# Kernel tuning notes

Measured on AMD Instinct MI355X. Metric: run time of the kernel, lower is better.

Reference implementation:

```python
import jax, jax.numpy as jnp
import numpy as np

EPS = 1e-5


def setup_inputs() -> dict:
    key = jax.random.key(0)
    ks = jax.random.split(key, 6)
    b, n, x_len, h_len = 128, 512, 512, 512
    fan_in = x_len + h_len
    std = float(np.sqrt(2.0 / fan_in))  # kaiming_normal_ for [h_len, x_len+h_len]
    X = jax.random.normal(ks[0], (b, n, x_len), dtype=jnp.float32)
    W_a = jax.random.normal(ks[1], (h_len, fan_in), dtype=jnp.float32) * std
    W_g = jax.random.normal(ks[2], (h_len, fan_in), dtype=jnp.float32) * std
    b_a = jax.random.normal(ks[3], (h_len,), dtype=jnp.float32) * 0.02
    b_g = jax.random.normal(ks[4], (h_len,), dtype=jnp.float32) * 0.02
    gamma = jnp.ones((h_len,), dtype=jnp.float32)
    beta = jnp.zeros((h_len,), dtype=jnp.float32)
    return {"X": X, "W_a": W_a, "W_g": W_g, "b_a": b_a, "b_g": b_g,
            "gamma": gamma, "beta": beta}


def _layernorm(x, gamma, beta):
    mu = jnp.mean(x, axis=-1, keepdims=True)
    var = jnp.mean(jnp.square(x - mu), axis=-1, keepdims=True)
    return (x - mu) * jax.lax.rsqrt(var + EPS) * gamma + beta


def reference(X, W_a, W_g, b_a, b_g, gamma, beta):
    # X: [b, n, x_len]; recurrent scan over the time axis n.
    b, n, x_len = X.shape
    h_len = W_a.shape[0]

    def step(h, x_t):
        cat = jnp.concatenate([h, x_t], axis=-1)          # [b, h+x]
        alpha = jax.nn.sigmoid(cat @ W_g.T + b_g)          # [b, h]
        a = cat @ W_a.T + b_a                              # [b, h]
        h_tilde = alpha * jnp.tanh(a) + (1.0 - alpha) * a  # affine blend
        h_new = _layernorm(h_tilde, gamma, beta)           # dropout = identity (eval)
        return h_new, h_new

    h0 = jnp.zeros((b, h_len), dtype=X.dtype)
    _, ys = jax.lax.scan(step, h0, jnp.swapaxes(X, 0, 1))  # ys: [n, b, h]
    return jnp.swapaxes(ys, 0, 1)                          # [b, n, h]
```

## Files before the change

kernel.cpp:

```cpp
#include <hip/hip_runtime.h>
#include <math.h>

typedef _Float16 f16;
typedef _Float16 f16x8 __attribute__((ext_vector_type(8)));
typedef float f32x4 __attribute__((ext_vector_type(4)));
typedef unsigned long long u64;
typedef unsigned u32;

union U32H2 { unsigned u; f16 h[2]; };
union UV4H8 { uint4 u; f16x8 h; f16 e[8]; };

#define LN_EPS 1e-5f

__device__ __forceinline__ void st_u64g(u64* p, u64 v) {
    __hip_atomic_store(p, v, __ATOMIC_RELAXED, __HIP_MEMORY_SCOPE_AGENT);
}
__device__ __forceinline__ u64 ld_u64g(const u64* p) {
    return __hip_atomic_load(p, __ATOMIC_RELAXED, __HIP_MEMORY_SCOPE_AGENT);
}

__global__ __launch_bounds__(256) void init_ex(u64* p, int n) {
    const int i = blockIdx.x * 256 + threadIdx.x;
    if (i < n) p[i] = 0ull;
}

__global__ __launch_bounds__(256) void pack_all(
    const float* __restrict__ Wa, const float* __restrict__ Wg,
    const float* __restrict__ gamma, uint4* __restrict__ WP,
    uint4* __restrict__ WPx)
{
    const int bid = blockIdx.x;
    const bool isH = (bid < 256);
    const int t = (isH ? bid : (bid - 256)) * 256 + threadIdx.x;
    const int lane = t & 63;
    const int kf = (t >> 6) & 15;
    const int tile = t >> 10;
    const float* W = (tile < 32) ? Wa : Wg;
    const int col = (tile & 31) * 16 + (lane & 15);
    const int k0 = kf * 32 + (lane >> 4) * 8;
    UV4H8 u;
    if (isH) {
        const float* src = W + (size_t)col * 1024 + k0;
#pragma unroll
        for (int j = 0; j < 8; ++j) u.e[j] = (f16)(src[j] * gamma[k0 + j]);
        WP[t] = u.u;
    } else {
        const float* src = W + (size_t)col * 1024 + 512 + k0;
#pragma unroll
        for (int j = 0; j < 8; ++j) u.e[j] = (f16)src[j];
        WPx[t] = u.u;
    }
}

__global__ __launch_bounds__(64) void precompute_consts(
    const float* __restrict__ Wa, const float* __restrict__ Wg,
    const float* __restrict__ gamma, const float* __restrict__ beta,
    float* __restrict__ Cvec)
{
    const int o = blockIdx.x;
    const int l = threadIdx.x;
    const float* wa = Wa + (size_t)o * 1024;
    const float* wg = Wg + (size_t)o * 1024;
    float ca = 0.f, ga = 0.f, cg = 0.f, gg = 0.f;
    for (int k = l; k < 512; k += 64) {
        const float bk = beta[k], gk = gamma[k], a = wa[k], g = wg[k];
        ca += a * bk; ga += a * gk; cg += g * bk; gg += g * gk;
    }
#pragma unroll
    for (int m = 1; m < 64; m <<= 1) {
        ca += __shfl_xor(ca, m); ga += __shfl_xor(ga, m);
        cg += __shfl_xor(cg, m); gg += __shfl_xor(gg, m);
    }
    if (l == 0) {
        Cvec[o] = ca; Cvec[512 + o] = ga; Cvec[1024 + o] = cg; Cvec[1536 + o] = gg;
    }
}

__global__ __launch_bounds__(512) void pgemm16(
    const float* __restrict__ X, const uint4* __restrict__ WPx,
    const float* __restrict__ ba, const float* __restrict__ bg,
    f16* __restrict__ Pah, f16* __restrict__ Pgh)
{
    __shared__ f16 As[2][128 * 64];
    const int tid = threadIdx.x;
    const int wv = tid >> 6, lane = tid & 63;
    const int bid = blockIdx.x;
    const int bn = bid & 7;
    const int bm = bid >> 3;
    const int m0 = bm * 128;
    const int tile = bn * 8 + wv;

    f16x8 Bf[16];
#pragma unroll
    for (int kf = 0; kf < 16; ++kf) {
        UV4H8 uu; uu.u = WPx[(size_t)(tile * 16 + kf) * 64 + lane];
        Bf[kf] = uu.h;
    }
    const int tcol = lane & 15;
    const float bias = (tile < 32) ? ba[tile * 16 + tcol]
                                   : bg[(tile - 32) * 16 + tcol];

    f32x4 acc[8];
#pragma unroll
    for (int mt = 0; mt < 8; ++mt) acc[mt] = (f32x4){0.f, 0.f, 0.f, 0.f};

    const int r = tid >> 2;
    const int c16 = (tid & 3) * 16;
    const int swzw = (r & 7) << 4;
    const int arow = lane & 15;
    const int swzr = (arow & 7) << 4;
    const int hi = (lane >> 4) * 16;
    const float* xrow = X + (size_t)(m0 + r) * 512 + c16;

    {
        const float4 v0 = *(const float4*)(xrow);
        const float4 v1 = *(const float4*)(xrow + 4);
        const float4 v2 = *(const float4*)(xrow + 8);
        const float4 v3 = *(const float4*)(xrow + 12);
        UV4H8 o0, o1;
        o0.e[0] = (f16)v0.x; o0.e[1] = (f16)v0.y; o0.e[2] = (f16)v0.z; o0.e[3] = (f16)v0.w;
        o0.e[4] = (f16)v1.x; o0.e[5] = (f16)v1.y; o0.e[6] = (f16)v1.z; o0.e[7] = (f16)v1.w;
        o1.e[0] = (f16)v2.x; o1.e[1] = (f16)v2.y; o1.e[2] = (f16)v2.z; o1.e[3] = (f16)v2.w;
        o1.e[4] = (f16)v3.x; o1.e[5] = (f16)v3.y; o1.e[6] = (f16)v3.z; o1.e[7] = (f16)v3.w;
        char* wb = (char*)&As[0][0] + r * 128;
        *(uint4*)(wb + ((c16 * 2) ^ swzw)) = o0.u;
        *(uint4*)(wb + ((c16 * 2 + 16) ^ swzw)) = o1.u;
    }
    __syncthreads();

    for (int kc = 0; kc < 8; ++kc) {
        const int cur = kc & 1;
        float4 v0, v1, v2, v3;
        if (kc < 7) {
            const float* src = xrow + (kc + 1) * 64;
            v0 = *(const float4*)(src);
            v1 = *(const float4*)(src + 4);
            v2 = *(const float4*)(src + 8);
            v3 = *(const float4*)(src + 12);
        }
#pragma unroll
        for (int mt = 0; mt < 8; ++mt) {
            const char* rbase = (const char*)&As[cur][0] + (mt * 16 + arow) * 128;
            const f16x8 Af0 = *(const f16x8*)(rbase + ((hi) ^ swzr));
            acc[mt] = __builtin_amdgcn_mfma_f32_16x16x32_f16(Af0, Bf[kc * 2], acc[mt], 0, 0, 0);
            const f16x8 Af1 = *(const f16x8*)(rbase + ((64 + hi) ^ swzr));
            acc[mt] = __builtin_amdgcn_mfma_f32_16x16x32_f16(Af1, Bf[kc * 2 + 1], acc[mt], 0, 0, 0);
        }
        if (kc < 7) {
            UV4H8 o0, o1;
            o0.e[0] = (f16)v0.x; o0.e[1] = (f16)v0.y; o0.e[2] = (f16)v0.z; o0.e[3] = (f16)v0.w;
            o0.e[4] = (f16)v1.x; o0.e[5] = (f16)v1.y; o0.e[6] = (f16)v1.z; o0.e[7] = (f16)v1.w;
            o1.e[0] = (f16)v2.x; o1.e[1] = (f16)v2.y; o1.e[2] = (f16)v2.z; o1.e[3] = (f16)v2.w;
            o1.e[4] = (f16)v3.x; o1.e[5] = (f16)v3.y; o1.e[6] = (f16)v3.z; o1.e[7] = (f16)v3.w;
            char* wb = (char*)&As[cur ^ 1][0] + r * 128;
            *(uint4*)(wb + ((c16 * 2) ^ swzw)) = o0.u;
            *(uint4*)(wb + ((c16 * 2 + 16) ^ swzw)) = o1.u;
        }
        __syncthreads();
    }

    const int drow = (lane >> 4) * 4;
    if (tile < 32) {
        const int col = tile * 16 + tcol;
#pragma unroll
        for (int mt = 0; mt < 8; ++mt)
#pragma unroll
            for (int i = 0; i < 4; ++i)
                Pah[(size_t)(m0 + mt * 16 + drow + i) * 512 + col] = (f16)(acc[mt][i] + bias);
    } else {
        const int col = (tile - 32) * 16 + tcol;
#pragma unroll
        for (int mt = 0; mt < 8; ++mt)
#pragma unroll
            for (int i = 0; i < 4; ++i)
                Pgh[(size_t)(m0 + mt * 16 + drow + i) * 512 + col] = (f16)(acc[mt][i] + bias);
    }
}

__global__ __launch_bounds__(512, 1) void scan14(
    const uint4* __restrict__ WP, const float* __restrict__ gamma,
    const float* __restrict__ beta, const float* __restrict__ Cvec,
    float* po, const f16* __restrict__ Pah, const f16* __restrict__ Pgh,
    u64* __restrict__ THex)
{
    __shared__ f16 hn[16][512];
    __shared__ float Dx[16][132];

    const int tid = threadIdx.x;
    const int wv = tid >> 6, lane = tid & 63;
    const int bid = blockIdx.x;
    const int rg = bid >> 3, cb = bid & 7;
    const int c0 = cb * 64, r0 = rg * 16;

    const int tile = (wv < 4) ? (cb * 4 + wv) : (32 + cb * 4 + (wv - 4));
    f16x8 Bf[16];
#pragma unroll
    for (int kf = 0; kf < 16; ++kf) {
        UV4H8 uu; uu.u = WP[(size_t)(tile * 16 + kf) * 64 + lane];
        Bf[kf] = uu.h;
    }

    for (int i = tid; i < 16 * 256; i += 512) ((unsigned*)hn)[i] = 0u;

    const int rb = tid >> 5, u = tid & 31;
    const int col0 = c0 + 2 * u;
    const float Ca0 = Cvec[col0],        Ca1 = Cvec[col0 + 1];
    const float Ga0 = Cvec[512 + col0],  Ga1 = Cvec[512 + col0 + 1];
    const float Cg0 = Cvec[1024 + col0], Cg1 = Cvec[1024 + col0 + 1];
    const float Gg0 = Cvec[1536 + col0], Gg1 = Cvec[1536 + col0 + 1];
    const float gm0 = gamma[col0], gm1 = gamma[col0 + 1];
    const float bt0 = beta[col0],  bt1 = beta[col0 + 1];

    const int arow = lane & 15;
    const int hi16 = (lane >> 4) * 16;
    const int swzr = (arow & 7) << 4;
    const int swzw = (rb & 7) << 4;
    const char* hrow_r = (const char*)&hn[arow][0];
    char* hrow_w = (char*)&hn[rb][0];
    const int dr = (lane >> 4) * 4;
    const int dc = wv * 16 + (lane & 15);
    const size_t row = (size_t)(r0 + rb);

    u64* pub0 = THex + ((size_t)0 * 8 + rg) * 4096 + (size_t)rb * 256 + cb * 32 + u;
    u64* pub1 = THex + ((size_t)1 * 8 + rg) * 4096 + (size_t)rb * 256 + cb * 32 + u;
    const u64* pol0 = THex + ((size_t)0 * 8 + rg) * 4096 + (size_t)rb * 256 + u;
    const u64* pol1 = THex + ((size_t)1 * 8 + rg) * 4096 + (size_t)rb * 256 + u;

    float ht0, ht1;
    {
        const size_t orow = (row * 512 + 0) * 512 + col0;
        U32H2 pa; pa.u = *(const unsigned*)(Pah + orow);
        U32H2 pg; pg.u = *(const unsigned*)(Pgh + orow);
        const float a0 = (float)pa.h[0], a1 = (float)pa.h[1];
        const float g0 = (float)pg.h[0], g1 = (float)pg.h[1];
        const float al0 = 1.f / (1.f + __expf(-g0));
        const float al1 = 1.f / (1.f + __expf(-g1));
        const float ac0 = fminf(fmaxf(a0, -15.f), 15.f);
        const float ac1 = fminf(fmaxf(a1, -15.f), 15.f);
        const float e0 = __expf(2.f * ac0), e1 = __expf(2.f * ac1);
        const float th0 = (e0 - 1.f) / (e0 + 1.f);
        const float th1 = (e1 - 1.f) / (e1 + 1.f);
        ht0 = al0 * (th0 - a0) + a0;
        ht1 = al1 * (th1 - a1) + a1;
        U32H2 hw; hw.h[0] = (f16)ht0; hw.h[1] = (f16)ht1;
        st_u64g(pub0, ((u64)1u << 32) | (u64)hw.u);
    }

    for (int t = 1; t < 512; ++t) {
        const unsigned tg = (unsigned)t;
        const u64* hp = ((t - 1) & 1) ? pol1 : pol0;
        const size_t orow = (row * 512 + (size_t)t) * 512 + col0;
        U32H2 pa; pa.u = *(const unsigned*)(Pah + orow);
        U32H2 pg; pg.u = *(const unsigned*)(Pgh + orow);

        u64 v[8];
        for (;;) {
#pragma unroll
            for (int i = 0; i < 8; ++i) v[i] = ld_u64g(hp + i * 32);
            bool ok = true;
#pragma unroll
            for (int i = 0; i < 8; ++i) ok &= ((unsigned)(v[i] >> 32) == tg);
            if (ok) break;
        }

        float s1 = 0.f, s2 = 0.f;
#pragma unroll
        for (int i = 0; i < 8; ++i) {
            U32H2 hh; hh.u = (unsigned)v[i];
            const float x0 = (float)hh.h[0], x1 = (float)hh.h[1];
            s1 += x0 + x1; s2 += x0 * x0 + x1 * x1;
            *(u32*)(hrow_w + ((128 * i + 4 * u) ^ swzw)) = (unsigned)v[i];
        }
        __syncthreads();

        f32x4 acc0 = {0.f, 0.f, 0.f, 0.f};
        f32x4 acc1 = {0.f, 0.f, 0.f, 0.f};
#pragma unroll
        for (int kf = 0; kf < 8; ++kf) {
            const f16x8 Af0 = *(const f16x8*)(hrow_r + ((kf * 64 + hi16) ^ swzr));
            acc0 = __builtin_amdgcn_mfma_f32_16x16x32_f16(Af0, Bf[kf], acc0, 0, 0, 0);
            const f16x8 Af1 = *(const f16x8*)(hrow_r + (((kf + 8) * 64 + hi16) ^ swzr));
            acc1 = __builtin_amdgcn_mfma_f32_16x16x32_f16(Af1, Bf[kf + 8], acc1, 0, 0, 0);
        }
        Dx[dr + 0][dc] = acc0[0] + acc1[0];
        Dx[dr + 1][dc] = acc0[1] + acc1[1];
        Dx[dr + 2][dc] = acc0[2] + acc1[2];
        Dx[dr + 3][dc] = acc0[3] + acc1[3];

#pragma unroll
        for (int m = 1; m < 32; m <<= 1) { s1 += __shfl_xor(s1, m); s2 += __shfl_xor(s2, m); }
        const float mu = s1 * (1.f / 512.f);
        const float var = s2 * (1.f / 512.f) - mu * mu;
        const float rs = rsqrtf(fmaxf(var, 0.f) + LN_EPS);
        const float murs = mu * rs;
        __syncthreads();

        const float a0 = rs * Dx[rb][2 * u]          - murs * Ga0 + Ca0 + (float)pa.h[0];
        const float a1 = rs * Dx[rb][2 * u + 1]      - murs * Ga1 + Ca1 + (float)pa.h[1];
        const float g0 = rs * Dx[rb][64 + 2 * u]     - murs * Gg0 + Cg0 + (float)pg.h[0];
        const float g1 = rs * Dx[rb][64 + 2 * u + 1] - murs * Gg1 + Cg1 + (float)pg.h[1];
        const float al0 = 1.f / (1.f + __expf(-g0));
        const float al1 = 1.f / (1.f + __expf(-g1));
        const float ac0 = fminf(fmaxf(a0, -15.f), 15.f);
        const float ac1 = fminf(fmaxf(a1, -15.f), 15.f);
        const float e0 = __expf(2.f * ac0), e1 = __expf(2.f * ac1);
        const float th0 = (e0 - 1.f) / (e0 + 1.f);
        const float th1 = (e1 - 1.f) / (e1 + 1.f);
        const float nt0 = al0 * (th0 - a0) + a0;
        const float nt1 = al1 * (th1 - a1) + a1;

        {
            U32H2 hw; hw.h[0] = (f16)nt0; hw.h[1] = (f16)nt1;
            st_u64g((t & 1) ? pub1 : pub0,
                    ((u64)(unsigned)(t + 1) << 32) | (u64)hw.u);
            po[orow - 512]     = (ht0 - mu) * rs * gm0 + bt0;
            po[orow - 512 + 1] = (ht1 - mu) * rs * gm1 + bt1;
            ht0 = nt0; ht1 = nt1;
        }
        __syncthreads();
    }

    {
        u64 v[8];
        for (;;) {
#pragma unroll
            for (int i = 0; i < 8; ++i) v[i] = ld_u64g(pol1 + i * 32);
            bool ok = true;
#pragma unroll
            for (int i = 0; i < 8; ++i) ok &= ((unsigned)(v[i] >> 32) == 512u);
            if (ok) break;
        }
        float s1 = 0.f, s2 = 0.f;
#pragma unroll
        for (int i = 0; i < 8; ++i) {
            U32H2 hh; hh.u = (unsigned)v[i];
            const float x0 = (float)hh.h[0], x1 = (float)hh.h[1];
            s1 += x0 + x1; s2 += x0 * x0 + x1 * x1;
        }
#pragma unroll
        for (int m = 1; m < 32; m <<= 1) { s1 += __shfl_xor(s1, m); s2 += __shfl_xor(s2, m); }
        const float mu = s1 * (1.f / 512.f);
        const float var = s2 * (1.f / 512.f) - mu * mu;
        const float rs = rsqrtf(fmaxf(var, 0.f) + LN_EPS);
        const size_t orow = (row * 512 + 511) * 512 + col0;
        po[orow]     = (ht0 - mu) * rs * gm0 + bt0;
        po[orow + 1] = (ht1 - mu) * rs * gm1 + bt1;
    }
}

extern "C" void kernel_launch(void* const* d_in, const int* in_sizes, int n_in,
                              void* d_out, int out_size, void* d_ws, size_t ws_size,
                              hipStream_t stream) {
    (void)in_sizes; (void)n_in; (void)out_size; (void)ws_size;
    const float* X     = (const float*)d_in[0];
    const float* Wa    = (const float*)d_in[1];
    const float* Wg    = (const float*)d_in[2];
    const float* ba    = (const float*)d_in[3];
    const float* bg    = (const float*)d_in[4];
    const float* gamma = (const float*)d_in[5];
    const float* beta  = (const float*)d_in[6];
    float* out = (float*)d_out;

    char* ws = (char*)d_ws;
    f16*    Pgh  = (f16*)ws;
    uint4*  WP   = (uint4*)(ws + 67108864);
    u64*    THex = (u64*)(ws + 68157440);
    float*  Cvec = (float*)(ws + 68681728);
    uint4*  WPx  = (uint4*)(ws + 68689920);
    f16*    Pah  = (f16*)(ws + 69738496);

    init_ex<<<dim3(256), dim3(256), 0, stream>>>(THex, 65536);
    pack_all<<<dim3(512), dim3(256), 0, stream>>>(Wa, Wg, gamma, WP, WPx);
    precompute_consts<<<dim3(512), dim3(64), 0, stream>>>(Wa, Wg, gamma, beta, Cvec);
    pgemm16<<<dim3(4096), dim3(512), 0, stream>>>(X, WPx, ba, bg, Pah, Pgh);

    void* args[] = { (void*)&WP, (void*)&gamma, (void*)&beta, (void*)&Cvec,
                     (void*)&out, (void*)&Pah, (void*)&Pgh, (void*)&THex };
    hipLaunchCooperativeKernel((const void*)scan14, dim3(64), dim3(512),
                               args, 0, stream);
}
```

Measured before the change: 1.453 ms.

## Fuse input-projection GEMM into scan kernel with producer-consumer overlap

Merges the separate input-projection GEMM and the recurrent scan into one cooperative kernel of 256 blocks. 64 blocks run the scan while 192 blocks compute the GEMM tiles in time-quarter order, and per-quarter counters with release/acquire atomics let the scan start once its first time slice is ready. This overlaps the GEMM with the latency-bound scan instead of running them back to back. The cost is extra polling and sync on the scan path, relaxed atomic loads for the P values, and GEMM blocks sharing the GPU with the scan blocks, which could slow the critical path.

```diff
diff --git a/kernel.cpp b/kernel.cpp
--- a/kernel.cpp
+++ b/kernel.cpp
@@ -9,6 +9,7 @@
 
 union U32H2 { unsigned u; f16 h[2]; };
 union UV4H8 { uint4 u; f16x8 h; f16 e[8]; };
+union H1 { unsigned short s; f16 h; };
 
 #define LN_EPS 1e-5f
 
@@ -17,6 +18,15 @@
 }
 __device__ __forceinline__ u64 ld_u64g(const u64* p) {
     return __hip_atomic_load(p, __ATOMIC_RELAXED, __HIP_MEMORY_SCOPE_AGENT);
+}
+__device__ __forceinline__ void st_u32g(u32* p, u32 v) {
+    __hip_atomic_store(p, v, __ATOMIC_RELAXED, __HIP_MEMORY_SCOPE_AGENT);
+}
+__device__ __forceinline__ u32 ld_u32g(const u32* p) {
+    return __hip_atomic_load(p, __ATOMIC_RELAXED, __HIP_MEMORY_SCOPE_AGENT);
+}
+__device__ __forceinline__ u32 ld_u32g_acq(const u32* p) {
+    return __hip_atomic_load(p, __ATOMIC_ACQUIRE, __HIP_MEMORY_SCOPE_AGENT);
 }
 
 __global__ __launch_bounds__(256) void init_ex(u64* p, int n) {
@@ -76,118 +86,127 @@
     }
 }
 
-__global__ __launch_bounds__(512) void pgemm16(
+__global__ __launch_bounds__(512, 1) void fused(
     const float* __restrict__ X, const uint4* __restrict__ WPx,
     const float* __restrict__ ba, const float* __restrict__ bg,
-    f16* __restrict__ Pah, f16* __restrict__ Pgh)
+    f16* __restrict__ Pah, f16* __restrict__ Pgh,
+    const uint4* __restrict__ WP, const float* __restrict__ gamma,
+    const float* __restrict__ beta, const float* __restrict__ Cvec,
+    float* po, u64* __restrict__ THex, u32* __restrict__ cnt)
 {
-    __shared__ f16 As[2][128 * 64];
+    __shared__ char smem[32768];
     const int tid = threadIdx.x;
     const int wv = tid >> 6, lane = tid & 63;
-    const int bid = blockIdx.x;
-    const int bn = bid & 7;
-    const int bm = bid >> 3;
-    const int m0 = bm * 128;
-    const int tile = bn * 8 + wv;
-
-    f16x8 Bf[16];
-#pragma unroll
-    for (int kf = 0; kf < 16; ++kf) {
-        UV4H8 uu; uu.u = WPx[(size_t)(tile * 16 + kf) * 64 + lane];
-        Bf[kf] = uu.h;
-    }
-    const int tcol = lane & 15;
-    const float bias = (tile < 32) ? ba[tile * 16 + tcol]
-                                   : bg[(tile - 32) * 16 + tcol];
-
-    f32x4 acc[8];
-#pragma unroll
-    for (int mt = 0; mt < 8; ++mt) acc[mt] = (f32x4){0.f, 0.f, 0.f, 0.f};
-
-    const int r = tid >> 2;
-    const int c16 = (tid & 3) * 16;
-    const int swzw = (r & 7) << 4;
-    const int arow = lane & 15;
-    const int swzr = (arow & 7) << 4;
-    const int hi = (lane >> 4) * 16;
-    const float* xrow = X + (size_t)(m0 + r) * 512 + c16;
-
-    {
-        const float4 v0 = *(const float4*)(xrow);
-        const float4 v1 = *(const float4*)(xrow + 4);
-        const float4 v2 = *(const float4*)(xrow + 8);
-        const float4 v3 = *(const float4*)(xrow + 12);
-        UV4H8 o0, o1;
-        o0.e[0] = (f16)v0.x; o0.e[1] = (f16)v0.y; o0.e[2] = (f16)v0.z; o0.e[3] = (f16)v0.w;
-        o0.e[4] = (f16)v1.x; o0.e[5] = (f16)v1.y; o0.e[6] = (f16)v1.z; o0.e[7] = (f16)v1.w;
-        o1.e[0] = (f16)v2.x; o1.e[1] = (f16)v2.y; o1.e[2] = (f16)v2.z; o1.e[3] = (f16)v2.w;
-        o1.e[4] = (f16)v3.x; o1.e[5] = (f16)v3.y; o1.e[6] = (f16)v3.z; o1.e[7] = (f16)v3.w;
-        char* wb = (char*)&As[0][0] + r * 128;
-        *(uint4*)(wb + ((c16 * 2) ^ swzw)) = o0.u;
-        *(uint4*)(wb + ((c16 * 2 + 16) ^ swzw)) = o1.u;
-    }
-    __syncthreads();
-
-    for (int kc = 0; kc < 8; ++kc) {
-        const int cur = kc & 1;
-        float4 v0, v1, v2, v3;
-        if (kc < 7) {
-            const float* src = xrow + (kc + 1) * 64;
-            v0 = *(const float4*)(src);
-            v1 = *(const float4*)(src + 4);
-            v2 = *(const float4*)(src + 8);
-            v3 = *(const float4*)(src + 12);
-        }
-#pragma unroll
-        for (int mt = 0; mt < 8; ++mt) {
-            const char* rbase = (const char*)&As[cur][0] + (mt * 16 + arow) * 128;
-            const f16x8 Af0 = *(const f16x8*)(rbase + ((hi) ^ swzr));
-            acc[mt] = __builtin_amdgcn_mfma_f32_16x16x32_f16(Af0, Bf[kc * 2], acc[mt], 0, 0, 0);
-            const f16x8 Af1 = *(const f16x8*)(rbase + ((64 + hi) ^ swzr));
-            acc[mt] = __builtin_amdgcn_mfma_f32_16x16x32_f16(Af1, Bf[kc * 2 + 1], acc[mt], 0, 0, 0);
-        }
-        if (kc < 7) {
-            UV4H8 o0, o1;
-            o0.e[0] = (f16)v0.x; o0.e[1] = (f16)v0.y; o0.e[2] = (f16)v0.z; o0.e[3] = (f16)v0.w;
-            o0.e[4] = (f16)v1.x; o0.e[5] = (f16)v1.y; o0.e[6] = (f16)v1.z; o0.e[7] = (f16)v1.w;
-            o1.e[0] = (f16)v2.x; o1.e[1] = (f16)v2.y; o1.e[2] = (f16)v2.z; o1.e[3] = (f16)v2.w;
-            o1.e[4] = (f16)v3.x; o1.e[5] = (f16)v3.y; o1.e[6] = (f16)v3.z; o1.e[7] = (f16)v3.w;
-            char* wb = (char*)&As[cur ^ 1][0] + r * 128;
-            *(uint4*)(wb + ((c16 * 2) ^ swzw)) = o0.u;
-            *(uint4*)(wb + ((c16 * 2 + 16) ^ swzw)) = o1.u;
-        }
-        __syncthreads();
-    }
-
-    const int drow = (lane >> 4) * 4;
-    if (tile < 32) {
-        const int col = tile * 16 + tcol;
-#pragma unroll
-        for (int mt = 0; mt < 8; ++mt)
-#pragma unroll
-            for (int i = 0; i < 4; ++i)
-                Pah[(size_t)(m0 + mt * 16 + drow + i) * 512 + col] = (f16)(acc[mt][i] + bias);
-    } else {
-        const int col = (tile - 32) * 16 + tcol;
-#pragma unroll
-        for (int mt = 0; mt < 8; ++mt)
-#pragma unroll
-            for (int i = 0; i < 4; ++i)
-                Pgh[(size_t)(m0 + mt * 16 + drow + i) * 512 + col] = (f16)(acc[mt][i] + bias);
-    }
-}
-
-__global__ __launch_bounds__(512, 1) void scan14(
-    const uint4* __restrict__ WP, const float* __restrict__ gamma,
-    const float* __restrict__ beta, const float* __restrict__ Cvec,
-    float* po, const f16* __restrict__ Pah, const f16* __restrict__ Pgh,
-    u64* __restrict__ THex)
-{
-    __shared__ f16 hn[16][512];
-    __shared__ float Dx[16][132];
-
-    const int tid = threadIdx.x;
-    const int wv = tid >> 6, lane = tid & 63;
+
+    if (blockIdx.x >= 64) {
+        f16* As0 = (f16*)smem;
+        f16* As1 = (f16*)(smem + 16384);
+        const int pb = blockIdx.x - 64;
+        const int tcol = lane & 15;
+        const int r = tid >> 2;
+        const int c16 = (tid & 3) * 16;
+        const int swzw = (r & 7) << 4;
+        const int arow = lane & 15;
+        const int swzr = (arow & 7) << 4;
+        const int hi = (lane >> 4) * 16;
+        const int drow = (lane >> 4) * 4;
+
+        for (int tile_id = pb; tile_id < 4096; tile_id += 192) {
+            const int tq = tile_id >> 10;
+            const int rem = tile_id & 1023;
+            const int rowb = rem >> 3;
+            const int bn = rem & 7;
+            const int m0 = (rowb * 4 + tq) * 128;
+            const int tile = bn * 8 + wv;
+
+            f16x8 Bf[16];
+#pragma unroll
+            for (int kf = 0; kf < 16; ++kf) {
+                UV4H8 uu; uu.u = WPx[(size_t)(tile * 16 + kf) * 64 + lane];
+                Bf[kf] = uu.h;
+            }
+            const float bias = (tile < 32) ? ba[tile * 16 + tcol]
+                                           : bg[(tile - 32) * 16 + tcol];
+            f32x4 acc[8];
+#pragma unroll
+            for (int mt = 0; mt < 8; ++mt) acc[mt] = (f32x4){0.f, 0.f, 0.f, 0.f};
+
+            const float* xrow = X + (size_t)(m0 + r) * 512 + c16;
+            {
+                const float4 v0 = *(const float4*)(xrow);
+                const float4 v1 = *(const float4*)(xrow + 4);
+                const float4 v2 = *(const float4*)(xrow + 8);
+                const float4 v3 = *(const float4*)(xrow + 12);
+                UV4H8 o0, o1;
+                o0.e[0] = (f16)v0.x; o0.e[1] = (f16)v0.y; o0.e[2] = (f16)v0.z; o0.e[3] = (f16)v0.w;
+                o0.e[4] = (f16)v1.x; o0.e[5] = (f16)v1.y; o0.e[6] = (f16)v1.z; o0.e[7] = (f16)v1.w;
+                o1.e[0] = (f16)v2.x; o1.e[1] = (f16)v2.y; o1.e[2] = (f16)v2.z; o1.e[3] = (f16)v2.w;
+                o1.e[4] = (f16)v3.x; o1.e[5] = (f16)v3.y; o1.e[6] = (f16)v3.z; o1.e[7] = (f16)v3.w;
+                char* wb = (char*)As0 + r * 128;
+                *(uint4*)(wb + ((c16 * 2) ^ swzw)) = o0.u;
+                *(uint4*)(wb + ((c16 * 2 + 16) ^ swzw)) = o1.u;
+            }
+            __syncthreads();
+
+            for (int kc = 0; kc < 8; ++kc) {
+                f16* curb = (kc & 1) ? As1 : As0;
+                f16* nxtb = (kc & 1) ? As0 : As1;
+                float4 v0, v1, v2, v3;
+                if (kc < 7) {
+                    const float* src = xrow + (kc + 1) * 64;
+                    v0 = *(const float4*)(src);
+                    v1 = *(const float4*)(src + 4);
+                    v2 = *(const float4*)(src + 8);
+                    v3 = *(const float4*)(src + 12);
+                }
+#pragma unroll
+                for (int mt = 0; mt < 8; ++mt) {
+                    const char* rbase = (const char*)curb + (mt * 16 + arow) * 128;
+                    const f16x8 Af0 = *(const f16x8*)(rbase + ((hi) ^ swzr));
+                    acc[mt] = __builtin_amdgcn_mfma_f32_16x16x32_f16(Af0, Bf[kc * 2], acc[mt], 0, 0, 0);
+                    const f16x8 Af1 = *(const f16x8*)(rbase + ((64 + hi) ^ swzr));
+                    acc[mt] = __builtin_amdgcn_mfma_f32_16x16x32_f16(Af1, Bf[kc * 2 + 1], acc[mt], 0, 0, 0);
+                }
+                if (kc < 7) {
+                    UV4H8 o0, o1;
+                    o0.e[0] = (f16)v0.x; o0.e[1] = (f16)v0.y; o0.e[2] = (f16)v0.z; o0.e[3] = (f16)v0.w;
+                    o0.e[4] = (f16)v1.x; o0.e[5] = (f16)v1.y; o0.e[6] = (f16)v1.z; o0.e[7] = (f16)v1.w;
+                    o1.e[0] = (f16)v2.x; o1.e[1] = (f16)v2.y; o1.e[2] = (f16)v2.z; o1.e[3] = (f16)v2.w;
+                    o1.e[4] = (f16)v3.x; o1.e[5] = (f16)v3.y; o1.e[6] = (f16)v3.z; o1.e[7] = (f16)v3.w;
+                    char* wb = (char*)nxtb + r * 128;
+                    *(uint4*)(wb + ((c16 * 2) ^ swzw)) = o0.u;
+                    *(uint4*)(wb + ((c16 * 2 + 16) ^ swzw)) = o1.u;
+                }
+                __syncthreads();
+            }
+
+            {
+                f16* Pdst = (tile < 32) ? Pah : Pgh;
+                const int colp = ((tile < 32) ? tile * 16 : (tile - 32) * 16) + tcol;
+#pragma unroll
+                for (int mt = 0; mt < 8; ++mt) {
+#pragma unroll
+                    for (int i = 0; i < 4; ++i) {
+                        H1 h; h.h = (f16)(acc[mt][i] + bias);
+                        const u32 other = __shfl_xor((u32)h.s, 1);
+                        if ((tcol & 1) == 0) {
+                            const u32 pr = (u32)h.s | (other << 16);
+                            st_u32g((u32*)(Pdst + (size_t)(m0 + mt * 16 + drow + i) * 512 + colp), pr);
+                        }
+                    }
+                }
+            }
+            __syncthreads();
+            if (tid == 0)
+                __hip_atomic_fetch_add(&cnt[(rowb >> 4) * 4 + tq], 1u,
+                                       __ATOMIC_RELEASE, __HIP_MEMORY_SCOPE_AGENT);
+        }
+        return;
+    }
+
+    f16 (*hn)[512] = (f16(*)[512])smem;
+    float (*Dx)[132] = (float(*)[132])(smem + 16384);
+
     const int bid = blockIdx.x;
     const int rg = bid >> 3, cb = bid & 7;
     const int c0 = cb * 64, r0 = rg * 16;
@@ -226,11 +245,16 @@
     const u64* pol0 = THex + ((size_t)0 * 8 + rg) * 4096 + (size_t)rb * 256 + u;
     const u64* pol1 = THex + ((size_t)1 * 8 + rg) * 4096 + (size_t)rb * 256 + u;
 
+    if (tid == 0) {
+        while (ld_u32g_acq(&cnt[rg * 4]) < 128u) __builtin_amdgcn_s_sleep(4);
+    }
+    __syncthreads();
+
     float ht0, ht1;
     {
         const size_t orow = (row * 512 + 0) * 512 + col0;
-        U32H2 pa; pa.u = *(const unsigned*)(Pah + orow);
-        U32H2 pg; pg.u = *(const unsigned*)(Pgh + orow);
+        U32H2 pa; pa.u = ld_u32g((const u32*)(Pah + orow));
+        U32H2 pg; pg.u = ld_u32g((const u32*)(Pgh + orow));
         const float a0 = (float)pa.h[0], a1 = (float)pa.h[1];
         const float g0 = (float)pg.h[0], g1 = (float)pg.h[1];
         const float al0 = 1.f / (1.f + __expf(-g0));
@@ -247,11 +271,18 @@
     }
 
     for (int t = 1; t < 512; ++t) {
+        if ((t & 127) == 0) {
+            if (tid == 0) {
+                const int ci = rg * 4 + (t >> 7);
+                while (ld_u32g_acq(&cnt[ci]) < 128u) __builtin_amdgcn_s_sleep(4);
+            }
+            __syncthreads();
+        }
         const unsigned tg = (unsigned)t;
         const u64* hp = ((t - 1) & 1) ? pol1 : pol0;
         const size_t orow = (row * 512 + (size_t)t) * 512 + col0;
-        U32H2 pa; pa.u = *(const unsigned*)(Pah + orow);
-        U32H2 pg; pg.u = *(const unsigned*)(Pgh + orow);
+        U32H2 pa; pa.u = ld_u32g((const u32*)(Pah + orow));
+        U32H2 pg; pg.u = ld_u32g((const u32*)(Pgh + orow));
 
         u64 v[8];
         for (;;) {
@@ -365,17 +396,19 @@
     f16*    Pgh  = (f16*)ws;
     uint4*  WP   = (uint4*)(ws + 67108864);
     u64*    THex = (u64*)(ws + 68157440);
-    float*  Cvec = (float*)(ws + 68681728);
-    uint4*  WPx  = (uint4*)(ws + 68689920);
-    f16*    Pah  = (f16*)(ws + 69738496);
-
-    init_ex<<<dim3(256), dim3(256), 0, stream>>>(THex, 65536);
+    u32*    cnt  = (u32*)(ws + 68681728);
+    float*  Cvec = (float*)(ws + 68682240);
+    uint4*  WPx  = (uint4*)(ws + 68690432);
+    f16*    Pah  = (f16*)(ws + 69739008);
+
+    init_ex<<<dim3(257), dim3(256), 0, stream>>>(THex, 65536 + 64);
     pack_all<<<dim3(512), dim3(256), 0, stream>>>(Wa, Wg, gamma, WP, WPx);
     precompute_consts<<<dim3(512), dim3(64), 0, stream>>>(Wa, Wg, gamma, beta, Cvec);
-    pgemm16<<<dim3(4096), dim3(512), 0, stream>>>(X, WPx, ba, bg, Pah, Pgh);
-
-    void* args[] = { (void*)&WP, (void*)&gamma, (void*)&beta, (void*)&Cvec,
-                     (void*)&out, (void*)&Pah, (void*)&Pgh, (void*)&THex };
-    hipLaunchCooperativeKernel((const void*)scan14, dim3(64), dim3(512),
+
+    void* args[] = { (void*)&X, (void*)&WPx, (void*)&ba, (void*)&bg,
+                     (void*)&Pah, (void*)&Pgh,
+                     (void*)&WP, (void*)&gamma, (void*)&beta, (void*)&Cvec,
+                     (void*)&out, (void*)&THex, (void*)&cnt };
+    hipLaunchCooperativeKernel((const void*)fused, dim3(256), dim3(512),
                                args, 0, stream);
 }
```

Measured after the change: 1.522 ms. +4.8%, slower.
